# Optimization experiments

Measured on AMD Instinct MI355X. Metric: run time of the kernel, lower is better.

## Reference

```python
import jax, jax.numpy as jnp
import numpy as np

B, H, N, L = 8, 128, 64, 8192
LOG_DT_MIN, LOG_DT_MAX = float(np.log(0.001)), float(np.log(0.1))


def setup_inputs() -> dict:
    key = jax.random.key(0)
    k_x, k_are, k_aim, k_c, k_dt = jax.random.split(key, 5)
    x = jax.random.normal(k_x, (B, H, L), dtype=jnp.float32)
    # A_re: negative real parts (clipped to <= -1e-4 in forward anyway)
    A_re = -jax.random.uniform(k_are, (H, N, 1), dtype=jnp.float32, minval=0.1, maxval=1.0)
    A_im = jax.random.normal(k_aim, (H, N, 1), dtype=jnp.float32) * float(np.pi)
    C = (0.5 ** 0.5) * jax.random.normal(k_c, (H, N, 2), dtype=jnp.float32)
    D = jnp.ones((1, H, 1), dtype=jnp.float32)
    u = jax.random.uniform(k_dt, (H, 1, 1), dtype=jnp.float32)
    log_delta = u * (LOG_DT_MAX - LOG_DT_MIN) + LOG_DT_MIN
    return {"x": x, "A_re": A_re, "A_im": A_im, "C": C, "D": D, "log_delta": log_delta}


def reference(x, A_re, A_im, C, D, log_delta):
    seq_len = x.shape[-1]
    # ---- S4D-ZOH kernel generation ----
    A = jnp.minimum(A_re, -1e-4) + 1j * A_im            # (H, N, 1) complex
    Cc = C[..., 0:1] + 1j * C[..., 1:2]                 # (H, N, 1) complex
    step = jnp.exp(log_delta)                           # (H, 1, 1)
    dA = step * A                                       # (H, N, 1)
    times = jnp.arange(seq_len, dtype=jnp.float32)[None, None, :]  # (1, 1, L)
    part = jnp.exp(times * dA)                          # (H, N, L)
    cons = (jnp.exp(dA) - 1.0) / A                      # (H, N, 1)
    K = jnp.sum(Cc * cons * part, axis=-2).real         # (H, L)
    # ---- causal conv via FFT (torch pads both to length 2L) ----
    n = seq_len + K.shape[-1]                           # 2L
    xd = jnp.fft.rfft(x, n=n, axis=-1)                  # (B, H, L+1)
    Kd = jnp.fft.rfft(K[None], n=n, axis=-1)            # (1, H, L+1)
    conv = jnp.fft.irfft(xd * Kd, n=n, axis=-1)[:, :, :seq_len]
    return conv + D * x
```

## Files before the change

### kernel.cpp

```cpp
#include <hip/hip_runtime.h>
#include <hip/hip_bf16.h>
#include <math.h>

#define B_ 8
#define H_ 128
#define N_ 64
#define L_ 8192
#define MCH 64
#define SCH (L_ / MCH)
#define EROW 136
#define NSEQ 2

#define LDS_Q     34816
#define LDS_P     51200
#define LDS_SEG   67584
#define LDS_KV    71680
#define LDS_TOTAL 71936

typedef __attribute__((ext_vector_type(8))) short bf16x8;
typedef __attribute__((ext_vector_type(4))) float f32x4;

__device__ __forceinline__ float bf2f(ushort s) { return __uint_as_float(((uint)s) << 16); }
__device__ __forceinline__ uint packbf2(float a, float b) {
    __hip_bfloat162 h = __float22bfloat162_rn(make_float2(a, b));
    union { __hip_bfloat162 h2; uint u; } cv; cv.h2 = h;
    return cv.u;
}
__device__ __forceinline__ bf16x8 pack_bf8(f32x4 a, f32x4 b) {
    union { uint u[4]; bf16x8 v; } r;
    r.u[0] = packbf2(a[0], a[1]); r.u[1] = packbf2(a[2], a[3]);
    r.u[2] = packbf2(b[0], b[1]); r.u[3] = packbf2(b[2], b[3]);
    return r.v;
}

__global__ __launch_bounds__(256, 2) void s4d_fused(
    const float* __restrict__ x,
    const float* __restrict__ A_re, const float* __restrict__ A_im,
    const float* __restrict__ Cp, const float* __restrict__ Dp,
    const float* __restrict__ log_delta,
    float* __restrict__ out)
{
    __shared__ __align__(16) char lds[LDS_TOTAL];
    ushort* EBUF = (ushort*)lds;
    char*   QTBL = lds + LDS_Q;
    char*   PTBL = lds + LDS_P;
    float*  seg  = (float*)(lds + LDS_SEG);
    float*  kv   = (float*)(lds + LDS_KV);

    const int h   = blockIdx.x % H_;
    const int bp  = blockIdx.x / H_;
    const int tid = threadIdx.x;
    const int w   = tid >> 6;
    const int lane = tid & 63;
    const int n16 = lane & 15, q = lane >> 4;
    const int n = lane, g = w;

    float are = fminf(A_re[h * N_ + n], -1e-4f);
    float aim = A_im[h * N_ + n];
    float step = expf(log_delta[h]);
    float dre = step * are, dim = step * aim;
    float er = expf(dre);
    float sd, cd; sincosf(dim, &sd, &cd);
    float rre = er * cd, rim = er * sd;
    float cre = Cp[(h * N_ + n) * 2 + 0];
    float cim = Cp[(h * N_ + n) * 2 + 1];
    float inv  = 1.0f / (are * are + aim * aim);
    float numr = rre - 1.0f, numi = rim;
    float consr = (numr * are + numi * aim) * inv;
    float consi = (numi * are - numr * aim) * inv;
    float wr = cre * consr - cim * consi;
    float wi = cre * consi + cim * consr;
    float dval = Dp[h];
    float m64r = rre, m64i = rim;
#pragma unroll
    for (int k = 0; k < 6; ++k) { float tr = m64r*m64r - m64i*m64i, ti = 2.f*m64r*m64i; m64r = tr; m64i = ti; }
    const float mr = m64r, mi = m64i;
    float m32r = mr, m32i = mi;
#pragma unroll
    for (int k = 0; k < 5; ++k) { float tr = m32r*m32r - m32i*m32i, ti = 2.f*m32r*m32i; m32r = tr; m32i = ti; }

    auto rp = [&](float d, float& pr, float& pi) {
        float ex = __expf(d * dre);
        float ang = d * dim;
        float s = __sinf(ang), c2 = __cosf(ang);
        pr = ex * c2; pi = ex * s;
    };

    const float* xs0 = x   + ((size_t)(2 * bp) * H_ + h) * L_;
    const float* xs1 = xs0 + (size_t)H_ * L_;
    float* op0 = out + ((size_t)(2 * bp) * H_ + h) * L_;
    float* op1 = op0 + (size_t)H_ * L_;

    bf16x8 xb0[2][2];
    f32x4 raw1[2][2][2];
#pragma unroll
    for (int ic = 0; ic < 2; ++ic) {
        int c = (2 * w + ic) * 16 + n16;
#pragma unroll
        for (int kc = 0; kc < 2; ++kc) {
            const float* p0 = xs0 + c * MCH + kc * 32 + q * 8;
            f32x4 f0 = __builtin_nontemporal_load((const f32x4*)p0);
            f32x4 f1 = __builtin_nontemporal_load((const f32x4*)p0 + 1);
            xb0[ic][kc] = pack_bf8(f0, f1);
            const float* p1 = xs1 + c * MCH + kc * 32 + q * 8;
            raw1[ic][kc][0] = __builtin_nontemporal_load((const f32x4*)p1);
            raw1[ic][kc][1] = __builtin_nontemporal_load((const f32x4*)p1 + 1);
        }
    }

    {
        uint qr[8], qi[8];
#pragma unroll
        for (int i = 0; i < 8; ++i) {
            int t0 = g * 16 + 2 * i;
            float ar0, ai0, ar1, ai1;
            rp((float)(63 - t0), ar0, ai0);
            rp((float)(62 - t0), ar1, ai1);
            qr[i] = packbf2(ar0, ar1);
            qi[i] = packbf2(ai0, ai1);
        }
        const int ra = 2 * n, rb = 2 * n + 1;
        const uint xa = (uint)(ra & 7) << 4, xbm = (uint)(rb & 7) << 4;
        *(uint4*)(QTBL + ((ra * 128 + g * 32     ) ^ xa))  = ((uint4*)qr)[0];
        *(uint4*)(QTBL + ((ra * 128 + g * 32 + 16) ^ xa))  = ((uint4*)qr)[1];
        *(uint4*)(QTBL + ((rb * 128 + g * 32     ) ^ xbm)) = ((uint4*)qi)[0];
        *(uint4*)(QTBL + ((rb * 128 + g * 32 + 16) ^ xbm)) = ((uint4*)qi)[1];
    }

    {
        float kvloc[16];
#pragma unroll
        for (int j = 0; j < 16; ++j) {
            float pr, pi; rp((float)(g * 16 + j), pr, pi);
            kvloc[j] = wr * pr - wi * pi;
        }
#pragma unroll
        for (int j = 0; j < 16; ++j) {
#pragma unroll
            for (int s = 1; s < 64; s <<= 1)
                kvloc[j] += __shfl_xor(kvloc[j], s, 64);
        }
#pragma unroll
        for (int j = 0; j < 16; ++j)
            if (n == j) kv[g * 16 + j] = kvloc[j];
    }

#pragma unroll
    for (int i = 0; i < 16; ++i) {
        int j = g * 16 + i;
        float pr, pi; rp((float)(j + 1), pr, pi);
        float ur = wr * pr - wi * pi;
        float ui = wr * pi + wi * pr;
        *(uint*)(PTBL + ((j * 256 + n * 4) ^ ((uint)(j & 7) << 4))) = packbf2(ur, -ui);
    }
    __syncthreads();

    bf16x8 tf[4][2];
#pragma unroll
    for (int rt = 0; rt < 4; ++rt) {
        int row = rt * 16 + n16;
        union { uint u[4]; bf16x8 v; } f0, f1;
#pragma unroll
        for (int kc = 0; kc < 2; ++kc) {
#pragma unroll
            for (int ki = 0; ki < 4; ++ki) {
                int t0 = kc * 32 + q * 8 + 2 * ki;
                int i0 = row - t0, i1 = i0 - 1;
                float v0 = kv[i0 & 63]; v0 = (i0 >= 0) ? v0 : 0.f; if (i0 == 0) v0 += dval;
                float v1 = kv[i1 & 63]; v1 = (i1 >= 0) ? v1 : 0.f; if (i1 == 0) v1 += dval;
                if (kc == 0) f0.u[ki] = packbf2(v0, v1); else f1.u[ki] = packbf2(v0, v1);
            }
        }
        tf[rt][0] = f0.v; tf[rt][1] = f1.v;
    }

    const uint xr = (uint)(n16 & 7) << 4;

    auto do_seq = [&](const bf16x8 (&xb)[2][2], int sb, float* op) {
#pragma unroll
        for (int rt = 0; rt < 8; ++rt) {
            int row = rt * 16 + n16;
            bf16x8 a0 = *(const bf16x8*)(QTBL + ((row * 128      + q * 16) ^ xr));
            bf16x8 a1 = *(const bf16x8*)(QTBL + ((row * 128 + 64 + q * 16) ^ xr));
#pragma unroll
            for (int ic = 0; ic < 2; ++ic) {
                f32x4 acc = {0.f, 0.f, 0.f, 0.f};
                acc = __builtin_amdgcn_mfma_f32_16x16x32_bf16(a0, xb[ic][0], acc, 0, 0, 0);
                acc = __builtin_amdgcn_mfma_f32_16x16x32_bf16(a1, xb[ic][1], acc, 0, 0, 0);
                int c = (2 * w + ic) * 16 + n16;
                uint2 st = make_uint2(packbf2(acc[0], acc[1]), packbf2(acc[2], acc[3]));
                *(uint2*)&EBUF[c * EROW + rt * 16 + q * 4] = st;
            }
        }

        float* sr_ = seg + sb * 512;
        float* si_ = sr_ + 256;
        {
            float sr = 0.f, si = 0.f;
#pragma unroll
            for (int j = 0; j < 32; ++j) {
                uint e = *(const uint*)&EBUF[(g * 32 + j) * EROW + 2 * n];
                float er2 = bf2f((ushort)(e & 0xffffu)), ei2 = bf2f((ushort)(e >> 16));
                float nr = er2 + mr * sr - mi * si;
                float ni = ei2 + mr * si + mi * sr;
                sr = nr; si = ni;
            }
            sr_[g * 64 + n] = sr; si_[g * 64 + n] = si;
        }

        f32x4 accT[4][2];
#pragma unroll
        for (int rt = 0; rt < 4; ++rt) {
#pragma unroll
            for (int ic = 0; ic < 2; ++ic) {
                f32x4 a = {0.f, 0.f, 0.f, 0.f};
                a = __builtin_amdgcn_mfma_f32_16x16x32_bf16(tf[rt][0], xb[ic][0], a, 0, 0, 0);
                a = __builtin_amdgcn_mfma_f32_16x16x32_bf16(tf[rt][1], xb[ic][1], a, 0, 0, 0);
                accT[rt][ic] = a;
            }
        }
        __syncthreads();

        {
            float pr2 = 0.f, pi2 = 0.f;
            for (int gp = 0; gp < g; ++gp) {
                float Er = sr_[gp * 64 + n], Ei = si_[gp * 64 + n];
                float nr = Er + m32r * pr2 - m32i * pi2;
                float ni = Ei + m32r * pi2 + m32i * pr2;
                pr2 = nr; pi2 = ni;
            }
            float sr = pr2, si = pi2;
#pragma unroll
            for (int j = 0; j < 32; ++j) {
                uint* ep = (uint*)&EBUF[(g * 32 + j) * EROW + 2 * n];
                uint e = *ep;
                float er2 = bf2f((ushort)(e & 0xffffu)), ei2 = bf2f((ushort)(e >> 16));
                *ep = packbf2(sr, si);
                float nr = er2 + mr * sr - mi * si;
                float ni = ei2 + mr * si + mi * sr;
                sr = nr; si = ni;
            }
        }

#pragma unroll
        for (int rt = 0; rt < 4; ++rt) {
            int row = rt * 16 + n16;
            bf16x8 p0 = *(const bf16x8*)(PTBL + ((row * 256       + q * 16) ^ xr));
            bf16x8 p1 = *(const bf16x8*)(PTBL + ((row * 256 +  64 + q * 16) ^ xr));
            bf16x8 p2 = *(const bf16x8*)(PTBL + ((row * 256 + 128 + q * 16) ^ xr));
            bf16x8 p3 = *(const bf16x8*)(PTBL + ((row * 256 + 192 + q * 16) ^ xr));
#pragma unroll
            for (int ic = 0; ic < 2; ++ic) {
                int c = (2 * w + ic) * 16 + n16;
                f32x4 accP = {0.f, 0.f, 0.f, 0.f};
                accP = __builtin_amdgcn_mfma_f32_16x16x32_bf16(p0,
                           *(const bf16x8*)&EBUF[c * EROW +       q * 8], accP, 0, 0, 0);
                accP = __builtin_amdgcn_mfma_f32_16x16x32_bf16(p1,
                           *(const bf16x8*)&EBUF[c * EROW +  32 + q * 8], accP, 0, 0, 0);
                accP = __builtin_amdgcn_mfma_f32_16x16x32_bf16(p2,
                           *(const bf16x8*)&EBUF[c * EROW +  64 + q * 8], accP, 0, 0, 0);
                accP = __builtin_amdgcn_mfma_f32_16x16x32_bf16(p3,
                           *(const bf16x8*)&EBUF[c * EROW +  96 + q * 8], accP, 0, 0, 0);
                f32x4 o;
                o[0] = accT[rt][ic][0] + accP[0];
                o[1] = accT[rt][ic][1] + accP[1];
                o[2] = accT[rt][ic][2] + accP[2];
                o[3] = accT[rt][ic][3] + accP[3];
                __builtin_nontemporal_store(o, (f32x4*)(op + c * MCH + rt * 16 + q * 4));
            }
        }
    };

    do_seq(xb0, 0, op0);

    bf16x8 xb1[2][2];
#pragma unroll
    for (int ic = 0; ic < 2; ++ic)
#pragma unroll
        for (int kc = 0; kc < 2; ++kc)
            xb1[ic][kc] = pack_bf8(raw1[ic][kc][0], raw1[ic][kc][1]);

    do_seq(xb1, 1, op1);
}

extern "C" void kernel_launch(void* const* d_in, const int* in_sizes, int n_in,
                              void* d_out, int out_size, void* d_ws, size_t ws_size,
                              hipStream_t stream)
{
    const float* x  = (const float*)d_in[0];
    const float* Ar = (const float*)d_in[1];
    const float* Ai = (const float*)d_in[2];
    const float* C  = (const float*)d_in[3];
    const float* D  = (const float*)d_in[4];
    const float* ld = (const float*)d_in[5];
    float* out = (float*)d_out;
    (void)d_ws; (void)ws_size;

    hipLaunchKernelGGL(s4d_fused, dim3(B_ * H_ / NSEQ), dim3(256), 0, stream,
                       x, Ar, Ai, C, D, ld, out);
}
```

Before: 103.8 us.

## Split chunk recurrence into two interleaved half-scans and defer P-table build

```diff
diff --git a/kernel.cpp b/kernel.cpp
--- a/kernel.cpp
+++ b/kernel.cpp
@@ -14,8 +14,8 @@
 #define LDS_Q     34816
 #define LDS_P     51200
 #define LDS_SEG   67584
-#define LDS_KV    71680
-#define LDS_TOTAL 71936
+#define LDS_KV    75776
+#define LDS_TOTAL 76032
 
 typedef __attribute__((ext_vector_type(8))) short bf16x8;
 typedef __attribute__((ext_vector_type(4))) float f32x4;
@@ -75,9 +75,6 @@
 #pragma unroll
     for (int k = 0; k < 6; ++k) { float tr = m64r*m64r - m64i*m64i, ti = 2.f*m64r*m64i; m64r = tr; m64i = ti; }
     const float mr = m64r, mi = m64i;
-    float m32r = mr, m32i = mi;
-#pragma unroll
-    for (int k = 0; k < 5; ++k) { float tr = m32r*m32r - m32i*m32i, ti = 2.f*m32r*m32i; m32r = tr; m32i = ti; }
 
     auto rp = [&](float d, float& pr, float& pi) {
         float ex = __expf(d * dre);
@@ -144,16 +141,11 @@
         for (int j = 0; j < 16; ++j)
             if (n == j) kv[g * 16 + j] = kvloc[j];
     }
-
-#pragma unroll
-    for (int i = 0; i < 16; ++i) {
-        int j = g * 16 + i;
-        float pr, pi; rp((float)(j + 1), pr, pi);
-        float ur = wr * pr - wi * pi;
-        float ui = wr * pi + wi * pr;
-        *(uint*)(PTBL + ((j * 256 + n * 4) ^ ((uint)(j & 7) << 4))) = packbf2(ur, -ui);
-    }
     __syncthreads();
+
+    float m16r = mr, m16i = mi;
+#pragma unroll
+    for (int k = 0; k < 4; ++k) { float tr = m16r*m16r - m16i*m16i, ti = 2.f*m16r*m16i; m16r = tr; m16i = ti; }
 
     bf16x8 tf[4][2];
 #pragma unroll
@@ -176,7 +168,7 @@
 
     const uint xr = (uint)(n16 & 7) << 4;
 
-    auto do_seq = [&](const bf16x8 (&xb)[2][2], int sb, float* op) {
+    auto do_seq = [&](const bf16x8 (&xb)[2][2], int sb, float* op, bool buildP) {
 #pragma unroll
         for (int rt = 0; rt < 8; ++rt) {
             int row = rt * 16 + n16;
@@ -193,19 +185,24 @@
             }
         }
 
-        float* sr_ = seg + sb * 512;
-        float* si_ = sr_ + 256;
+        float* sr_ = seg + sb * 1024;
+        float* si_ = sr_ + 512;
         {
-            float sr = 0.f, si = 0.f;
-#pragma unroll
-            for (int j = 0; j < 32; ++j) {
-                uint e = *(const uint*)&EBUF[(g * 32 + j) * EROW + 2 * n];
-                float er2 = bf2f((ushort)(e & 0xffffu)), ei2 = bf2f((ushort)(e >> 16));
-                float nr = er2 + mr * sr - mi * si;
-                float ni = ei2 + mr * si + mi * sr;
-                sr = nr; si = ni;
-            }
-            sr_[g * 64 + n] = sr; si_[g * 64 + n] = si;
+            float sAr = 0.f, sAi = 0.f, sBr = 0.f, sBi = 0.f;
+#pragma unroll
+            for (int j = 0; j < 16; ++j) {
+                uint eA = *(const uint*)&EBUF[(g * 32 + j     ) * EROW + 2 * n];
+                uint eB = *(const uint*)&EBUF[(g * 32 + 16 + j) * EROW + 2 * n];
+                float eAr = bf2f((ushort)(eA & 0xffffu)), eAi = bf2f((ushort)(eA >> 16));
+                float eBr = bf2f((ushort)(eB & 0xffffu)), eBi = bf2f((ushort)(eB >> 16));
+                float nAr = eAr + mr * sAr - mi * sAi;
+                float nAi = eAi + mr * sAi + mi * sAr;
+                float nBr = eBr + mr * sBr - mi * sBi;
+                float nBi = eBi + mr * sBi + mi * sBr;
+                sAr = nAr; sAi = nAi; sBr = nBr; sBi = nBi;
+            }
+            sr_[(2 * g    ) * 64 + n] = sAr; si_[(2 * g    ) * 64 + n] = sAi;
+            sr_[(2 * g + 1) * 64 + n] = sBr; si_[(2 * g + 1) * 64 + n] = sBi;
         }
 
         f32x4 accT[4][2];
@@ -219,26 +216,45 @@
                 accT[rt][ic] = a;
             }
         }
+
+        if (buildP) {
+#pragma unroll
+            for (int i = 0; i < 16; ++i) {
+                int j = g * 16 + i;
+                float pr, pi; rp((float)(j + 1), pr, pi);
+                float ur = wr * pr - wi * pi;
+                float ui = wr * pi + wi * pr;
+                *(uint*)(PTBL + ((j * 256 + n * 4) ^ ((uint)(j & 7) << 4))) = packbf2(ur, -ui);
+            }
+        }
         __syncthreads();
 
         {
             float pr2 = 0.f, pi2 = 0.f;
-            for (int gp = 0; gp < g; ++gp) {
-                float Er = sr_[gp * 64 + n], Ei = si_[gp * 64 + n];
-                float nr = Er + m32r * pr2 - m32i * pi2;
-                float ni = Ei + m32r * pi2 + m32i * pr2;
+            for (int s = 0; s < 2 * g; ++s) {
+                float Er = sr_[s * 64 + n], Ei = si_[s * 64 + n];
+                float nr = Er + m16r * pr2 - m16i * pi2;
+                float ni = Ei + m16r * pi2 + m16i * pr2;
                 pr2 = nr; pi2 = ni;
             }
-            float sr = pr2, si = pi2;
-#pragma unroll
-            for (int j = 0; j < 32; ++j) {
-                uint* ep = (uint*)&EBUF[(g * 32 + j) * EROW + 2 * n];
-                uint e = *ep;
-                float er2 = bf2f((ushort)(e & 0xffffu)), ei2 = bf2f((ushort)(e >> 16));
-                *ep = packbf2(sr, si);
-                float nr = er2 + mr * sr - mi * si;
-                float ni = ei2 + mr * si + mi * sr;
-                sr = nr; si = ni;
+            float sAr = pr2, sAi = pi2;
+            float Gr = sr_[(2 * g) * 64 + n], Gi = si_[(2 * g) * 64 + n];
+            float sBr = Gr + m16r * pr2 - m16i * pi2;
+            float sBi = Gi + m16r * pi2 + m16i * pr2;
+#pragma unroll
+            for (int j = 0; j < 16; ++j) {
+                uint* epA = (uint*)&EBUF[(g * 32 + j     ) * EROW + 2 * n];
+                uint* epB = (uint*)&EBUF[(g * 32 + 16 + j) * EROW + 2 * n];
+                uint eA = *epA, eB = *epB;
+                float eAr = bf2f((ushort)(eA & 0xffffu)), eAi = bf2f((ushort)(eA >> 16));
+                float eBr = bf2f((ushort)(eB & 0xffffu)), eBi = bf2f((ushort)(eB >> 16));
+                *epA = packbf2(sAr, sAi);
+                *epB = packbf2(sBr, sBi);
+                float nAr = eAr + mr * sAr - mi * sAi;
+                float nAi = eAi + mr * sAi + mi * sAr;
+                float nBr = eBr + mr * sBr - mi * sBi;
+                float nBi = eBi + mr * sBi + mi * sBr;
+                sAr = nAr; sAi = nAi; sBr = nBr; sBi = nBi;
             }
         }
 
@@ -271,7 +287,7 @@
         }
     };
 
-    do_seq(xb0, 0, op0);
+    do_seq(xb0, 0, op0, true);
 
     bf16x8 xb1[2][2];
 #pragma unroll
@@ -280,7 +296,7 @@
         for (int kc = 0; kc < 2; ++kc)
             xb1[ic][kc] = pack_bf8(raw1[ic][kc][0], raw1[ic][kc][1]);
 
-    do_seq(xb1, 1, op1);
+    do_seq(xb1, 1, op1, false);
 }
 
 extern "C" void kernel_launch(void* const* d_in, const int* in_sizes, int n_in,
```

New measurement: 103.2 us. About the same (-0.5%).
